# Kernel tuning notes

Measured on AMD Instinct MI355X. Metric: run time of the kernel, lower is better.

The kernel has to match this reference:

```python
import jax, jax.numpy as jnp
import numpy as np

B, F, V, C = 2048, 2048, 50257, 50257


def setup_inputs() -> dict:
    key = jax.random.key(0)
    ks = jax.random.split(key, 16)
    s = 0.02  # init scale
    return {
        "X": jax.random.randint(ks[0], (B,), 0, V),
        "h": jax.random.normal(ks[1], (B, F), jnp.float32),
        "c": jax.random.normal(ks[2], (B, F), jnp.float32),
        "emb": jax.random.normal(ks[3], (V, F), jnp.float32) * s,
        "Wf": jax.random.normal(ks[4], (2 * F, F), jnp.float32) * s,
        "bf": jnp.zeros((F,), jnp.float32),
        "Wi": jax.random.normal(ks[5], (2 * F, F), jnp.float32) * s,
        "bi": jnp.zeros((F,), jnp.float32),
        "Wig": jax.random.normal(ks[6], (2 * F, F), jnp.float32) * s,
        "big": jnp.zeros((F,), jnp.float32),
        "Wog": jax.random.normal(ks[7], (2 * F, F), jnp.float32) * s,
        "bog": jnp.zeros((F,), jnp.float32),
        "Wcls": jax.random.normal(ks[8], (F, C), jnp.float32) * s,
        "bcls": jnp.zeros((C,), jnp.float32),
    }


def reference(X, h, c, emb, Wf, bf, Wi, bi, Wig, big, Wog, bog, Wcls, bcls):
    # Embedding lookup: [B] -> [B, F]
    x = emb[X]
    xh = jnp.concatenate([x, h], axis=-1)  # [B, 2F]
    # Fuse the four gate GEMMs into one [B,2F] @ [2F,4F] matmul.
    Wg = jnp.concatenate([Wf, Wig, Wog, Wi], axis=1)   # [2F, 4F]
    bg = jnp.concatenate([bf, big, bog, bi], axis=0)   # [4F]
    gates = xh @ Wg + bg                                # [B, 4F]
    f_pre, ig_pre, og_pre, g_pre = jnp.split(gates, 4, axis=-1)
    forget_gate = jax.nn.sigmoid(f_pre)
    input_gate = jax.nn.sigmoid(ig_pre)
    output_gate = jax.nn.sigmoid(og_pre)
    g = jnp.tanh(g_pre)
    c_new = forget_gate * c + input_gate * g
    h_new = output_gate * jnp.tanh(c_new)
    y = h_new @ Wcls + bcls  # [B, C]
    return (y, h_new, c_new)
```

## Files before the change

kernel.cpp:

```cpp
#include <hip/hip_runtime.h>
#include <hip/hip_bf16.h>

typedef __attribute__((ext_vector_type(4))) float f32x4;
typedef __attribute__((ext_vector_type(8))) short short8;
typedef __attribute__((ext_vector_type(8))) unsigned short ushort8;
typedef __attribute__((ext_vector_type(4))) unsigned short u16x4;
typedef float f4a __attribute__((ext_vector_type(4), aligned(4)));

__device__ __forceinline__ unsigned short f2bf(float f) {
  unsigned int u = __float_as_uint(f);
  u += 0x7fffu + ((u >> 16) & 1u);
  return (unsigned short)(u >> 16);
}

#define BARRIER do { asm volatile("" ::: "memory"); __builtin_amdgcn_s_barrier(); asm volatile("" ::: "memory"); } while(0)
#define LGKM    asm volatile("s_waitcnt lgkmcnt(0)" ::: "memory")
#define VMW(n)  asm volatile("s_waitcnt vmcnt(" #n ")" ::: "memory")

__global__ __launch_bounds__(256) void k_build_xh(
    const int* __restrict__ X, const float* __restrict__ h,
    const float* __restrict__ emb, unsigned short* __restrict__ xh) {
  int b = blockIdx.x;
  int tid = threadIdx.x;
  int j0 = tid * 16;
  const float* src;
  if (j0 < 2048) {
    int xb = X[b];
    src = emb + (size_t)xb * 2048 + j0;
  } else {
    src = h + (size_t)b * 2048 + (j0 - 2048);
  }
  unsigned short* dst = xh + (size_t)b * 4096 + j0;
#pragma unroll
  for (int half = 0; half < 2; ++half) {
    float4 f0 = *(const float4*)(src + half * 8);
    float4 f1 = *(const float4*)(src + half * 8 + 4);
    ushort8 o;
    o[0] = f2bf(f0.x); o[1] = f2bf(f0.y); o[2] = f2bf(f0.z); o[3] = f2bf(f0.w);
    o[4] = f2bf(f1.x); o[5] = f2bf(f1.y); o[6] = f2bf(f1.z); o[7] = f2bf(f1.w);
    *(ushort8*)(dst + half * 8) = o;
  }
}

__global__ __launch_bounds__(256) void k_cvt_wg(
    const float* __restrict__ W0, const float* __restrict__ W1,
    const float* __restrict__ W2, const float* __restrict__ W3,
    unsigned short* __restrict__ WT) {
  const int g = blockIdx.z;
  const float* W = (g == 0) ? W0 : (g == 1) ? W1 : (g == 2) ? W2 : W3;
  int tid = threadIdx.x, lane = tid & 63, w = tid >> 6;
  int n0 = blockIdx.x * 64, k0 = blockIdx.y * 64;
  int nb = n0 + 4 * (lane & 15);
  int kb = k0 + w * 16 + 4 * (lane >> 4);
  float v[4][4];
#pragma unroll
  for (int r = 0; r < 4; ++r) {
    f4a x = *(const f4a*)(W + (size_t)(kb + r) * 2048 + nb);
    v[r][0] = x.x; v[r][1] = x.y; v[r][2] = x.z; v[r][3] = x.w;
  }
#pragma unroll
  for (int e = 0; e < 4; ++e) {
    int col = nb + e;
    int row = ((col >> 6) << 8) + g * 64 + (col & 63);
    u16x4 o;
    o[0] = f2bf(v[0][e]); o[1] = f2bf(v[1][e]);
    o[2] = f2bf(v[2][e]); o[3] = f2bf(v[3][e]);
    *(u16x4*)(WT + (size_t)row * 4096 + kb) = o;
  }
}

__global__ __launch_bounds__(256) void k_cvt_t(
    const float* __restrict__ W, unsigned short* __restrict__ WT,
    int K, int Nin, int ldo) {
  int tid = threadIdx.x;
  int lane = tid & 63, w = tid >> 6;
  int n0 = blockIdx.x * 64, k0 = blockIdx.y * 64;
  int nb = n0 + 4 * (lane & 15);
  int kb = k0 + w * 16 + 4 * (lane >> 4);
  float v[4][4];
  if (nb + 3 < Nin) {
#pragma unroll
    for (int r = 0; r < 4; ++r) {
      f4a x = *(const f4a*)(W + (size_t)(kb + r) * Nin + nb);
      v[r][0] = x.x; v[r][1] = x.y; v[r][2] = x.z; v[r][3] = x.w;
    }
  } else {
#pragma unroll
    for (int r = 0; r < 4; ++r)
#pragma unroll
      for (int e = 0; e < 4; ++e)
        v[r][e] = (nb + e < Nin) ? W[(size_t)(kb + r) * Nin + nb + e] : 0.f;
  }
#pragma unroll
  for (int e = 0; e < 4; ++e) {
    if (nb + e < Nin) {
      u16x4 o;
      o[0] = f2bf(v[0][e]); o[1] = f2bf(v[1][e]);
      o[2] = f2bf(v[2][e]); o[3] = f2bf(v[3][e]);
      *(u16x4*)(WT + (size_t)(nb + e) * ldo + kb) = o;
    }
  }
}

struct EpiP {
  const float *c, *b0, *b1, *b2, *b3;
  float *hnew, *cnew;
  unsigned short* hnbf;
};

__device__ __forceinline__ short8 ld_fragA(const unsigned char* smem, int buf, int half,
                                           int row_local, int ks, int lane) {
  unsigned kbyte = (unsigned)(ks * 64 + ((lane >> 4) << 4));
  unsigned off = (unsigned)(buf * 2 + half) * 16384u + (unsigned)row_local * 128u
               + (kbyte ^ (((unsigned)row_local & 7u) << 4));
  return *(const short8*)(smem + off);
}
__device__ __forceinline__ short8 ld_fragB(const unsigned char* smem, int buf, int half,
                                           int col_local, int ks, int lane) {
  unsigned kbyte = (unsigned)(ks * 64 + ((lane >> 4) << 4));
  unsigned off = 65536u + (unsigned)(buf * 2 + half) * 16384u + (unsigned)col_local * 128u
               + (kbyte ^ (((unsigned)col_local & 7u) << 4));
  return *(const short8*)(smem + off);
}

template <int EPI>
__global__ __launch_bounds__(512, 1) void k_gemm256(
    const unsigned short* __restrict__ A, const unsigned short* __restrict__ Bt,
    const float* __restrict__ bias, float* __restrict__ C,
    int N, int K, int lda, int ldb, int rowmaxB, EpiP P) {
  __shared__ __align__(16) unsigned char smem[131072];
  const int tid = threadIdx.x, lane = tid & 63, wid = tid >> 6;
  const int wr = wid >> 2, wc = wid & 3;

  int nwg = gridDim.x * gridDim.y;
  int o = blockIdx.y * gridDim.x + blockIdx.x;
  int q = nwg >> 3;
  int s = (o & 7) * q + (o >> 3);
  const int mrow0 = (s & 7) * 256;
  const int ncol0 = (s >> 3) * 256;

  const int NKT = K >> 6;

  unsigned vA[2], vB[2][2];
#pragma unroll
  for (int i = 0; i < 2; ++i) {
    unsigned phys = (unsigned)(i * 512 + tid) * 16u;
    unsigned logi = phys ^ (((phys >> 7) & 7u) << 4);
    unsigned r = logi >> 7;
    unsigned kbe = (logi & 127u) >> 1;
    vA[i] = r * (unsigned)lda + kbe;
#pragma unroll
    for (int hh = 0; hh < 2; ++hh) {
      int br = ncol0 + hh * 128 + (int)r;
      br = (br > rowmaxB) ? rowmaxB : br;
      vB[hh][i] = (unsigned)br * (unsigned)ldb + kbe;
    }
  }
  const unsigned short* Ab0 = A + (size_t)mrow0 * lda;
  const unsigned short* Ab1 = Ab0 + (size_t)128 * lda;

  f32x4 acc[8][4];
#pragma unroll
  for (int m = 0; m < 8; ++m)
#pragma unroll
    for (int n = 0; n < 4; ++n) acc[m][n] = {0.f, 0.f, 0.f, 0.f};

  short8 a_frag[4][2], b_frag[2][2][2];

#define STG(baseptr, v, ldsoff) __builtin_amdgcn_global_load_lds( \
    (const __attribute__((address_space(1))) void*)((baseptr) + (v)), \
    (__attribute__((address_space(3))) void*)(smem + (ldsoff)), 16, 0, 0)
#define ST_A(buf, hh, t) do { const unsigned short* _b = (hh ? Ab1 : Ab0) + (size_t)(t) * 64; \
    STG(_b, vA[0], (unsigned)((buf) * 2 + (hh)) * 16384u + (unsigned)(wid * 1024)); \
    STG(_b, vA[1], (unsigned)((buf) * 2 + (hh)) * 16384u + (unsigned)(8192 + wid * 1024)); } while (0)
#define ST_B(buf, hh, t) do { const unsigned short* _b = Bt + (size_t)(t) * 64; \
    STG(_b, vB[hh][0], 65536u + (unsigned)((buf) * 2 + (hh)) * 16384u + (unsigned)(wid * 1024)); \
    STG(_b, vB[hh][1], 65536u + (unsigned)((buf) * 2 + (hh)) * 16384u + (unsigned)(8192 + wid * 1024)); } while (0)
#define RD_A(buf, mh) do { _Pragma("unroll") for (int mm = 0; mm < 4; ++mm) { int rl = (mh) * 64 + mm * 16 + (lane & 15); _Pragma("unroll") for (int ks = 0; ks < 2; ++ks) a_frag[mm][ks] = ld_fragA(smem, (buf), wr, rl, ks, lane); } } while (0)
#define RD_B(buf, nh) do { _Pragma("unroll") for (int nn = 0; nn < 2; ++nn) { int cl = (wc & 1) * 64 + (nh) * 32 + nn * 16 + (lane & 15); _Pragma("unroll") for (int ks = 0; ks < 2; ++ks) b_frag[nh][nn][ks] = ld_fragB(smem, (buf), (wc >> 1), cl, ks, lane); } } while (0)
#define MF(mh, nh) do { __builtin_amdgcn_s_setprio(1); _Pragma("unroll") for (int mm = 0; mm < 4; ++mm) _Pragma("unroll") for (int nn = 0; nn < 2; ++nn) _Pragma("unroll") for (int ks = 0; ks < 2; ++ks) acc[(mh) * 4 + mm][(nh) * 2 + nn] = __builtin_amdgcn_mfma_f32_16x16x32_bf16(a_frag[mm][ks], b_frag[(nh)][nn][ks], acc[(mh) * 4 + mm][(nh) * 2 + nn], 0, 0, 0); __builtin_amdgcn_s_setprio(0); } while (0)

  ST_A(0, 0, 0); ST_A(0, 1, 0); ST_B(0, 0, 0); ST_B(0, 1, 0);
  ST_B(1, 0, 1); ST_B(1, 1, 1);
  VMW(4); BARRIER;

  for (int t0 = 0; t0 + 3 < NKT; t0 += 2) {
    RD_A(0, 0); RD_B(0, 0); ST_A(1, 0, t0 + 1);
    BARRIER; LGKM; MF(0, 0); BARRIER;
    RD_B(0, 1); ST_A(1, 1, t0 + 1);
    BARRIER; LGKM; MF(0, 1); BARRIER;
    RD_A(0, 1); ST_B(0, 0, t0 + 2);
    BARRIER; LGKM; MF(1, 1); BARRIER;
    ST_B(0, 1, t0 + 2); VMW(4);
    BARRIER; LGKM; MF(1, 0); BARRIER;
    RD_A(1, 0); RD_B(1, 0); ST_A(0, 0, t0 + 2);
    BARRIER; LGKM; MF(0, 0); BARRIER;
    RD_B(1, 1); ST_A(0, 1, t0 + 2);
    BARRIER; LGKM; MF(0, 1); BARRIER;
    RD_A(1, 1); ST_B(1, 0, t0 + 3);
    BARRIER; LGKM; MF(1, 1); BARRIER;
    ST_B(1, 1, t0 + 3); VMW(4);
    BARRIER; LGKM; MF(1, 0); BARRIER;
  }

  {
    const int t1 = NKT - 1;
    RD_A(0, 0); RD_B(0, 0); ST_A(1, 0, t1);
    BARRIER; LGKM; MF(0, 0); BARRIER;
    RD_B(0, 1); ST_A(1, 1, t1);
    BARRIER; LGKM; MF(0, 1); BARRIER;
    RD_A(0, 1);
    BARRIER; LGKM; MF(1, 1); BARRIER;
    VMW(0);
    BARRIER; LGKM; MF(1, 0); BARRIER;
    RD_A(1, 0); RD_B(1, 0);
    BARRIER; LGKM; MF(0, 0); BARRIER;
    RD_B(1, 1);
    BARRIER; LGKM; MF(0, 1); BARRIER;
    RD_A(1, 1);
    BARRIER; LGKM; MF(1, 1); BARRIER;
    BARRIER; LGKM; MF(1, 0); BARRIER;
  }

  __syncthreads();

  if constexpr (EPI == 0) {
    float* wlds = (float*)(smem + (unsigned)wid * 16384u);
    const int gcol = ncol0 + wc * 64 + lane;
    const bool cok = (gcol < N);
    const float bv = (bias != nullptr && cok) ? bias[gcol] : 0.f;
#pragma unroll
    for (int mh = 0; mh < 2; ++mh) {
#pragma unroll
      for (int mm = 0; mm < 4; ++mm)
#pragma unroll
        for (int nn = 0; nn < 4; ++nn)
#pragma unroll
          for (int r = 0; r < 4; ++r) {
            int row = mm * 16 + ((lane >> 4) << 2) + r;
            int colv = nn * 16 + (lane & 15);
            int cs = (colv + ((row >> 2) & 3) * 16) & 63;
            wlds[row * 64 + cs] = acc[mh * 4 + mm][nn][r];
          }
#pragma unroll 8
      for (int row = 0; row < 64; ++row) {
        int cs = (lane + ((row >> 2) & 3) * 16) & 63;
        float v = wlds[row * 64 + cs] + bv;
        int grow = mrow0 + wr * 128 + mh * 64 + row;
        if (cok) C[(size_t)grow * N + gcol] = v;
      }
    }
  } else {
    float* ep = (float*)(smem + (unsigned)wr * 65536u);
    const int lt = (wid & 3) * 64 + lane;
    const int jj = lt & 63;
    const int rh = lt >> 6;
    const int gjj = (ncol0 >> 2) + jj;
    const float bf_ = P.b0[gjj], big_ = P.b1[gjj], bog_ = P.b2[gjj], bi_ = P.b3[gjj];
#pragma unroll
    for (int mh = 0; mh < 2; ++mh) {
#pragma unroll
      for (int mm = 0; mm < 4; ++mm)
#pragma unroll
        for (int nn = 0; nn < 4; ++nn)
#pragma unroll
          for (int r = 0; r < 4; ++r) {
            int row = mm * 16 + ((lane >> 4) << 2) + r;
            int colv = nn * 16 + (lane & 15);
            int cs = (colv + ((row >> 2) & 3) * 16) & 63;
            ep[row * 256 + wc * 64 + cs] = acc[mh * 4 + mm][nn][r];
          }
      __syncthreads();
#pragma unroll
      for (int rr = 0; rr < 16; ++rr) {
        int row = rh * 16 + rr;
        int rot = (jj + ((row >> 2) & 3) * 16) & 63;
        float g0 = ep[row * 256 +   0 + rot];
        float g1 = ep[row * 256 +  64 + rot];
        float g2 = ep[row * 256 + 128 + rot];
        float g3 = ep[row * 256 + 192 + rot];
        int grow = mrow0 + wr * 128 + mh * 64 + row;
        size_t off = (size_t)grow * 2048 + gjj;
        float fg = 1.f / (1.f + expf(-(g0 + bf_)));
        float ig = 1.f / (1.f + expf(-(g1 + big_)));
        float og = 1.f / (1.f + expf(-(g2 + bog_)));
        float gt = tanhf(g3 + bi_);
        float cn = fg * P.c[off] + ig * gt;
        float hn = og * tanhf(cn);
        P.cnew[off] = cn;
        P.hnew[off] = hn;
        P.hnbf[off] = f2bf(hn);
      }
      __syncthreads();
    }
  }
#undef STG
#undef ST_A
#undef ST_B
#undef RD_A
#undef RD_B
#undef MF
}

__global__ __launch_bounds__(256) void k_gemm_tail(
    const unsigned short* __restrict__ A, const unsigned short* __restrict__ Bt,
    const float* __restrict__ bias, float* __restrict__ C,
    int N, int K, int lda, int ncol_base) {
  __shared__ unsigned short As[128 * 32];
  __shared__ unsigned short Bs[128 * 32];
  const int tid = threadIdx.x;
  const int lane = tid & 63;
  const int wid = tid >> 6;

  int nwg = gridDim.x * gridDim.y;
  int o = blockIdx.y * gridDim.x + blockIdx.x;
  int q = nwg >> 3;
  int s = (o & 7) * q + (o >> 3);
  const int mrow0 = (s / gridDim.x) * 128;
  const int ncol0 = ncol_base + (s % gridDim.x) * 128;

  f32x4 acc[4][4];
#pragma unroll
  for (int m = 0; m < 4; ++m)
#pragma unroll
    for (int n = 0; n < 4; ++n) acc[m][n] = {0.f, 0.f, 0.f, 0.f};

  const int wr = wid >> 1, wc = wid & 1;
  const int brow0 = wr * 64, bcol0 = wc * 64;

  int a_off[4], b_off[4];
#pragma unroll
  for (int m = 0; m < 4; ++m)
    a_off[m] = (brow0 + m * 16 + (lane & 15)) * 32 + ((lane >> 4) << 3);
#pragma unroll
  for (int n = 0; n < 4; ++n)
    b_off[n] = (bcol0 + n * 16 + (lane & 15)) * 32 + ((lane >> 4) << 3);

  for (int k0 = 0; k0 < K; k0 += 32) {
#pragma unroll
    for (int i = 0; i < 2; ++i) {
      int slot = i * 256 + tid;
      int r = slot >> 2, ck = slot & 3;
      unsigned short* la = As + (size_t)(i * 256 + wid * 64) * 8;
      unsigned short* lb = Bs + (size_t)(i * 256 + wid * 64) * 8;
      const unsigned short* ga = A + (size_t)(mrow0 + r) * lda + k0 + ck * 8;
      const unsigned short* gb = Bt + (size_t)(ncol0 + r) * K + k0 + ck * 8;
      __builtin_amdgcn_global_load_lds(
          (const __attribute__((address_space(1))) void*)ga,
          (__attribute__((address_space(3))) void*)la, 16, 0, 0);
      __builtin_amdgcn_global_load_lds(
          (const __attribute__((address_space(1))) void*)gb,
          (__attribute__((address_space(3))) void*)lb, 16, 0, 0);
    }
    __syncthreads();
    short8 af[4], bfr[4];
#pragma unroll
    for (int m = 0; m < 4; ++m) af[m] = *(const short8*)&As[a_off[m]];
#pragma unroll
    for (int n = 0; n < 4; ++n) bfr[n] = *(const short8*)&Bs[b_off[n]];
#pragma unroll
    for (int m = 0; m < 4; ++m)
#pragma unroll
      for (int n = 0; n < 4; ++n)
        acc[m][n] = __builtin_amdgcn_mfma_f32_16x16x32_bf16(af[m], bfr[n], acc[m][n], 0, 0, 0);
    __syncthreads();
  }

#pragma unroll
  for (int n = 0; n < 4; ++n) {
    int col = ncol0 + bcol0 + n * 16 + (lane & 15);
    if (col < N) {
      float bv = bias ? bias[col] : 0.f;
#pragma unroll
      for (int m = 0; m < 4; ++m) {
        int row0 = mrow0 + brow0 + m * 16 + ((lane >> 4) << 2);
        f32x4 v = acc[m][n];
#pragma unroll
        for (int r = 0; r < 4; ++r)
          C[(size_t)(row0 + r) * N + col] = v[r] + bv;
      }
    }
  }
}

extern "C" void kernel_launch(void* const* d_in, const int* in_sizes, int n_in,
                              void* d_out, int out_size, void* d_ws, size_t ws_size,
                              hipStream_t stream) {
  const int B = 2048, F = 2048, Ccls = 50257;
  const int NT = 50304;
  const int*   X    = (const int*)d_in[0];
  const float* h    = (const float*)d_in[1];
  const float* c    = (const float*)d_in[2];
  const float* emb  = (const float*)d_in[3];
  const float* Wf   = (const float*)d_in[4];
  const float* bf   = (const float*)d_in[5];
  const float* Wi   = (const float*)d_in[6];
  const float* bi   = (const float*)d_in[7];
  const float* Wig  = (const float*)d_in[8];
  const float* big  = (const float*)d_in[9];
  const float* Wog  = (const float*)d_in[10];
  const float* bog  = (const float*)d_in[11];
  const float* Wcls = (const float*)d_in[12];
  const float* bcls = (const float*)d_in[13];

  float* y    = (float*)d_out;
  float* hnew = y + (size_t)B * Ccls;
  float* cnew = hnew + (size_t)B * F;

  char* ws = (char*)d_ws;
  unsigned short* hnbf  = (unsigned short*)ws;
  unsigned short* xh    = (unsigned short*)(ws + 8388608);
  unsigned short* WgT   = (unsigned short*)(ws + 25165824);
  unsigned short* WclsT = (unsigned short*)(ws + 8388608);

  EpiP pz{nullptr, nullptr, nullptr, nullptr, nullptr, nullptr, nullptr, nullptr};

  k_build_xh<<<B, 256, 0, stream>>>(X, h, emb, xh);

  k_cvt_wg<<<dim3(32, 64, 4), 256, 0, stream>>>(Wf, Wig, Wog, Wi, WgT);

  EpiP pl{c, bf, big, bog, bi, hnew, cnew, hnbf};
  k_gemm256<1><<<dim3(8, 32), 512, 0, stream>>>(
      xh, WgT, nullptr, nullptr, 8192, 4096, 4096, 4096, 8191, pl);

  k_cvt_t<<<dim3(786, 32), 256, 0, stream>>>(Wcls, WclsT, 2048, Ccls, 2048);

  k_gemm256<0><<<dim3(8, 192), 512, 0, stream>>>(
      hnbf, WclsT, bcls, y, Ccls, 2048, 2048, 2048, NT - 1, pz);

  k_gemm_tail<<<dim3(9, 16), 256, 0, stream>>>(
      hnbf, WclsT, bcls, y, Ccls, 2048, 2048, 49152);
}
```

Measured before the change: 783.6 us.

## Prefetch A tiles a full k-step ahead with split lo/hi staging in GEMM pipeline

Restructures the GEMM main loop's global-to-LDS staging. A tiles are now loaded two k-steps ahead into the buffer just consumed, split by row halves (lo/hi) instead of by M-halves, and the prologue preloads both buffers for A and B. The goal is deeper prefetch so global-load latency is hidden behind more MFMA work. In exchange more loads are in flight (vmcnt raised to 8), and the timing of buffer reuse against the reads must remain correct.

```diff
diff --git a/kernel.cpp b/kernel.cpp
--- a/kernel.cpp
+++ b/kernel.cpp
@@ -170,9 +170,14 @@
 #define STG(baseptr, v, ldsoff) __builtin_amdgcn_global_load_lds( \
     (const __attribute__((address_space(1))) void*)((baseptr) + (v)), \
     (__attribute__((address_space(3))) void*)(smem + (ldsoff)), 16, 0, 0)
-#define ST_A(buf, hh, t) do { const unsigned short* _b = (hh ? Ab1 : Ab0) + (size_t)(t) * 64; \
-    STG(_b, vA[0], (unsigned)((buf) * 2 + (hh)) * 16384u + (unsigned)(wid * 1024)); \
-    STG(_b, vA[1], (unsigned)((buf) * 2 + (hh)) * 16384u + (unsigned)(8192 + wid * 1024)); } while (0)
+#define ST_A_LO(buf, t) do { const unsigned short* _b0 = Ab0 + (size_t)(t) * 64; \
+    const unsigned short* _b1 = Ab1 + (size_t)(t) * 64; \
+    STG(_b0, vA[0], (unsigned)((buf) * 2 + 0) * 16384u + (unsigned)(wid * 1024)); \
+    STG(_b1, vA[0], (unsigned)((buf) * 2 + 1) * 16384u + (unsigned)(wid * 1024)); } while (0)
+#define ST_A_HI(buf, t) do { const unsigned short* _b0 = Ab0 + (size_t)(t) * 64; \
+    const unsigned short* _b1 = Ab1 + (size_t)(t) * 64; \
+    STG(_b0, vA[1], (unsigned)((buf) * 2 + 0) * 16384u + (unsigned)(8192 + wid * 1024)); \
+    STG(_b1, vA[1], (unsigned)((buf) * 2 + 1) * 16384u + (unsigned)(8192 + wid * 1024)); } while (0)
 #define ST_B(buf, hh, t) do { const unsigned short* _b = Bt + (size_t)(t) * 64; \
     STG(_b, vB[hh][0], 65536u + (unsigned)((buf) * 2 + (hh)) * 16384u + (unsigned)(wid * 1024)); \
     STG(_b, vB[hh][1], 65536u + (unsigned)((buf) * 2 + (hh)) * 16384u + (unsigned)(8192 + wid * 1024)); } while (0)
@@ -180,34 +185,33 @@
 #define RD_B(buf, nh) do { _Pragma("unroll") for (int nn = 0; nn < 2; ++nn) { int cl = (wc & 1) * 64 + (nh) * 32 + nn * 16 + (lane & 15); _Pragma("unroll") for (int ks = 0; ks < 2; ++ks) b_frag[nh][nn][ks] = ld_fragB(smem, (buf), (wc >> 1), cl, ks, lane); } } while (0)
 #define MF(mh, nh) do { __builtin_amdgcn_s_setprio(1); _Pragma("unroll") for (int mm = 0; mm < 4; ++mm) _Pragma("unroll") for (int nn = 0; nn < 2; ++nn) _Pragma("unroll") for (int ks = 0; ks < 2; ++ks) acc[(mh) * 4 + mm][(nh) * 2 + nn] = __builtin_amdgcn_mfma_f32_16x16x32_bf16(a_frag[mm][ks], b_frag[(nh)][nn][ks], acc[(mh) * 4 + mm][(nh) * 2 + nn], 0, 0, 0); __builtin_amdgcn_s_setprio(0); } while (0)
 
-  ST_A(0, 0, 0); ST_A(0, 1, 0); ST_B(0, 0, 0); ST_B(0, 1, 0);
-  ST_B(1, 0, 1); ST_B(1, 1, 1);
-  VMW(4); BARRIER;
+  ST_A_LO(0, 0); ST_A_HI(0, 0); ST_B(0, 0, 0); ST_B(0, 1, 0);
+  ST_A_LO(1, 1); ST_A_HI(1, 1); ST_B(1, 0, 1); ST_B(1, 1, 1);
+  VMW(8); BARRIER;
 
   for (int t0 = 0; t0 + 3 < NKT; t0 += 2) {
-    RD_A(0, 0); RD_B(0, 0); ST_A(1, 0, t0 + 1);
+    RD_A(0, 0); RD_B(0, 0);
     BARRIER; LGKM; MF(0, 0); BARRIER;
-    RD_B(0, 1); ST_A(1, 1, t0 + 1);
+    RD_B(0, 1); ST_A_LO(0, t0 + 2);
     BARRIER; LGKM; MF(0, 1); BARRIER;
-    RD_A(0, 1); ST_B(0, 0, t0 + 2);
+    RD_A(0, 1); ST_B(0, 0, t0 + 2); ST_B(0, 1, t0 + 2);
     BARRIER; LGKM; MF(1, 1); BARRIER;
-    ST_B(0, 1, t0 + 2); VMW(4);
+    ST_A_HI(0, t0 + 2); VMW(8);
     BARRIER; LGKM; MF(1, 0); BARRIER;
-    RD_A(1, 0); RD_B(1, 0); ST_A(0, 0, t0 + 2);
+    RD_A(1, 0); RD_B(1, 0);
     BARRIER; LGKM; MF(0, 0); BARRIER;
-    RD_B(1, 1); ST_A(0, 1, t0 + 2);
+    RD_B(1, 1); ST_A_LO(1, t0 + 3);
     BARRIER; LGKM; MF(0, 1); BARRIER;
-    RD_A(1, 1); ST_B(1, 0, t0 + 3);
+    RD_A(1, 1); ST_B(1, 0, t0 + 3); ST_B(1, 1, t0 + 3);
     BARRIER; LGKM; MF(1, 1); BARRIER;
-    ST_B(1, 1, t0 + 3); VMW(4);
+    ST_A_HI(1, t0 + 3); VMW(8);
     BARRIER; LGKM; MF(1, 0); BARRIER;
   }
 
   {
-    const int t1 = NKT - 1;
-    RD_A(0, 0); RD_B(0, 0); ST_A(1, 0, t1);
+    RD_A(0, 0); RD_B(0, 0);
     BARRIER; LGKM; MF(0, 0); BARRIER;
-    RD_B(0, 1); ST_A(1, 1, t1);
+    RD_B(0, 1);
     BARRIER; LGKM; MF(0, 1); BARRIER;
     RD_A(0, 1);
     BARRIER; LGKM; MF(1, 1); BARRIER;
@@ -295,7 +299,8 @@
     }
   }
 #undef STG
-#undef ST_A
+#undef ST_A_LO
+#undef ST_A_HI
 #undef ST_B
 #undef RD_A
 #undef RD_B
```

Measured after the change: 787.7 us, median of 2. About the same (+0.5%).
